# Kernel tuning notes

Hardware: AMD Instinct MI355X
Metric: run time of the kernel (lower is better)

Reference implementation:

```python
import jax, jax.numpy as jnp
import numpy as np

HEADS = 8
DIM_HEAD = 64

def setup_inputs() -> dict:
    key = jax.random.key(0)
    k1, k2, k3 = jax.random.split(key, 3)
    B, L, D = 8, 4096, 512
    hidden = HEADS * DIM_HEAD  # 512
    x = jax.random.normal(k1, (B, L, D), dtype=jnp.float32)
    # Conv1d(kernel_size=1) weights, squeezed to 2D matrices
    Wqkv = jax.random.normal(k2, (3 * hidden, D), dtype=jnp.float32) * (1.0 / np.sqrt(D))
    Wout = jax.random.normal(k3, (D, hidden), dtype=jnp.float32) * (1.0 / np.sqrt(hidden))
    bout = jnp.zeros((D,), dtype=jnp.float32)
    return {"x": x, "Wqkv": Wqkv, "Wout": Wout, "bout": bout}

def reference(x, Wqkv, Wout, bout):
    B, L, D = x.shape
    H, C = HEADS, DIM_HEAD
    # pointwise conv == linear over channel dim: (b, 3*H*C, l)
    qkv = jnp.einsum('bld,od->bol', x, Wqkv)
    qkv = qkv.reshape(B, 3, H, C, L)  # channel split order: (qkv, heads, c)
    q, k, v = qkv[:, 0], qkv[:, 1], qkv[:, 2]  # each (b, h, c, l)
    k = jax.nn.softmax(k, axis=-1)   # softmax over sequence
    q = jax.nn.softmax(q, axis=-2)   # softmax over feature dim (q_norm=True)
    context = jnp.einsum('bhdn,bhen->bhde', k, v)   # (b,h,c,c)
    out = jnp.einsum('bhde,bhdn->bhen', context, q)  # (b,h,c,l)
    out = out.reshape(B, H * C, L)
    y = jnp.einsum('bcl,dc->bld', out, Wout) + bout  # to_out + permute back
    return y
```

## Files before the change

### kernel.cpp

```cpp
#include <hip/hip_runtime.h>

#define L 4096
#define D 512
#define NCH 16

typedef __bf16 bf16x8 __attribute__((ext_vector_type(8)));
typedef float  f32x4  __attribute__((ext_vector_type(4)));

__device__ __forceinline__ void load_lds16(const void* g, void* l) {
    __builtin_amdgcn_global_load_lds(
        (const __attribute__((address_space(1))) void*)g,
        (__attribute__((address_space(3))) void*)l, 16, 0, 0);
}

__device__ __forceinline__ void barrier_mem() {
    asm volatile("" ::: "memory");
    __builtin_amdgcn_s_barrier();
    asm volatile("" ::: "memory");
}

#define NX8  (8 * 4096 * 512 / 8)
#define NW18 (1536 * 512 / 8)
#define NW28 (512 * 512 / 8)
__global__ __launch_bounds__(256) void convert_all(const float* __restrict__ x,
                                                   const float* __restrict__ Wq,
                                                   const float* __restrict__ Wo,
                                                   __bf16* __restrict__ dst) {
    int i = blockIdx.x * 256 + threadIdx.x;
    if (i >= NX8 + NW18 + NW28) return;
    const float* s;
    if (i < NX8)             s = x  + (size_t)i * 8;
    else if (i < NX8 + NW18) s = Wq + (size_t)(i - NX8) * 8;
    else                     s = Wo + (size_t)(i - NX8 - NW18) * 8;
    float4 a = ((const float4*)s)[0], b = ((const float4*)s)[1];
    bf16x8 o = {(__bf16)a.x, (__bf16)a.y, (__bf16)a.z, (__bf16)a.w,
                (__bf16)b.x, (__bf16)b.y, (__bf16)b.z, (__bf16)b.w};
    *(bf16x8*)(dst + (size_t)i * 8) = o;
}

template <int M, int N, int K, typename CT>
__global__ __launch_bounds__(256, 2) void gemm_bf16_256x128(
    const __bf16* __restrict__ A, size_t aStride,
    const __bf16* __restrict__ B, size_t bStride,
    CT* __restrict__ C, size_t cStride,
    const float* __restrict__ bias) {
    __shared__ __align__(16) __bf16 sA[3][256 * 32];
    __shared__ __align__(16) __bf16 sB[3][128 * 32];
    constexpr int NQ = K / 32;
    const int b  = blockIdx.z;
    const int m0 = blockIdx.y * 256;
    const int n0 = blockIdx.x * 128;
    const int t    = threadIdx.x;
    const int wave = t >> 6, lane = t & 63;
    const int wm = (wave >> 1) * 128;
    const int wn = (wave & 1) * 64;
    const int fr = lane & 15, g = lane >> 4;
    const __bf16* Ab = A + (size_t)b * aStride + (size_t)m0 * K;
    const __bf16* Bb = B + (size_t)b * bStride + (size_t)n0 * K;
    CT* Cb = C + (size_t)b * cStride;

    f32x4 acc[8][4];
#pragma unroll
    for (int i = 0; i < 8; i++)
#pragma unroll
        for (int j = 0; j < 4; j++) acc[i][j] = (f32x4)(0.0f);

    auto stageA = [&](int q, __bf16* slot) {
#pragma unroll
        for (int it = 0; it < 4; ++it) {
            const int gi = it * 256 + t;
            const int row = gi >> 2, cc = gi & 3;
            const int scc = cc ^ ((row >> 1) & 3);
            load_lds16(Ab + (size_t)row * K + q * 32 + scc * 8, slot + gi * 8);
        }
    };
    auto stageB = [&](int q, __bf16* slot) {
#pragma unroll
        for (int it = 0; it < 2; ++it) {
            const int gi = it * 256 + t;
            const int row = gi >> 2, cc = gi & 3;
            const int scc = cc ^ ((row >> 1) & 3);
            load_lds16(Bb + (size_t)row * K + q * 32 + scc * 8, slot + gi * 8);
        }
    };
    auto rdFrag = [&](const __bf16* slot, int rowbase) -> bf16x8 {
        const int row = rowbase + fr;
        return *(const bf16x8*)&slot[row * 32 + ((g ^ ((row >> 1) & 3)) * 8)];
    };

    stageB(0, sB[0]); stageA(0, sA[0]);
    stageB(1, sB[1]); stageA(1, sA[1]);

    for (int q = 0; q < NQ; ++q) {
        const int sl = q % 3;
        if (q < NQ - 1) asm volatile("s_waitcnt vmcnt(6)" ::: "memory");
        else            asm volatile("s_waitcnt vmcnt(0)" ::: "memory");
        barrier_mem();
        if (q + 2 < NQ) {
            const int ss = (q + 2) % 3;
            stageB(q + 2, sB[ss]);
            stageA(q + 2, sA[ss]);
        }
        bf16x8 fB[4], fA[8];
#pragma unroll
        for (int j = 0; j < 4; ++j) fB[j] = rdFrag(sB[sl], wn + j * 16);
#pragma unroll
        for (int i = 0; i < 8; ++i) fA[i] = rdFrag(sA[sl], wm + i * 16);
        asm volatile("s_waitcnt lgkmcnt(0)" ::: "memory");
        __builtin_amdgcn_sched_barrier(0);
        __builtin_amdgcn_s_setprio(1);
#pragma unroll
        for (int i = 0; i < 8; ++i)
#pragma unroll
            for (int j = 0; j < 4; ++j)
                acc[i][j] = __builtin_amdgcn_mfma_f32_16x16x32_bf16(
                    fA[i], fB[j], acc[i][j], 0, 0, 0);
        __builtin_amdgcn_s_setprio(0);
    }

    const int rb = g * 4;
    float bv[4];
#pragma unroll
    for (int j = 0; j < 4; ++j) bv[j] = bias ? bias[n0 + wn + j * 16 + fr] : 0.0f;
#pragma unroll
    for (int i = 0; i < 8; ++i) {
#pragma unroll
        for (int r = 0; r < 4; ++r) {
            const int m = m0 + wm + i * 16 + rb + r;
            CT* rowp = Cb + (size_t)m * N + n0 + wn + fr;
#pragma unroll
            for (int j = 0; j < 4; ++j)
                rowp[j * 16] = (CT)(acc[i][j][r] + bv[j]);
        }
    }
}

__global__ __launch_bounds__(256) void kstats(const __bf16* __restrict__ qkv,
                                              float2* __restrict__ stats) {
    const int r = blockIdx.x;
    const int b = r >> 9, hc = r & 511;
    const __bf16* row = qkv + (size_t)b * 1536 * L + (size_t)(512 + hc) * L;
    __shared__ float sred[4];
    const int t = threadIdx.x;
    const bf16x8* p = (const bf16x8*)row;
    bf16x8 c0 = p[t * 2], c1 = p[t * 2 + 1];
    float v[16];
    float m = -1e30f;
#pragma unroll
    for (int j = 0; j < 8; j++) {
        v[j] = (float)c0[j];
        v[8 + j] = (float)c1[j];
    }
#pragma unroll
    for (int j = 0; j < 16; j++) m = fmaxf(m, v[j]);
#pragma unroll
    for (int off = 32; off > 0; off >>= 1) m = fmaxf(m, __shfl_down(m, off, 64));
    if ((t & 63) == 0) sred[t >> 6] = m;
    __syncthreads();
    const float m4 = fmaxf(fmaxf(sred[0], sred[1]), fmaxf(sred[2], sred[3]));
    float s = 0.f;
#pragma unroll
    for (int j = 0; j < 16; j++) s += __expf(v[j] - m4);
#pragma unroll
    for (int off = 32; off > 0; off >>= 1) s += __shfl_down(s, off, 64);
    __syncthreads();
    if ((t & 63) == 0) sred[t >> 6] = s;
    __syncthreads();
    if (t == 0) {
        const float stot = sred[0] + sred[1] + sred[2] + sred[3];
        stats[r] = make_float2(m4, 1.0f / stot);
    }
}

#define SKS 264
__global__ __launch_bounds__(256) void context_mfma(const __bf16* __restrict__ qkv,
                                                    const float2* __restrict__ stats,
                                                    float* __restrict__ ctxp) {
    __shared__ __align__(16) __bf16 smem[2 * 64 * SKS];
    __shared__ float smax[64];
    __bf16* sk = smem;
    __bf16* sv = smem + 64 * SKS;
    const int chunk = blockIdx.x;
    const int bh = blockIdx.y;
    const int b = bh >> 3, h = bh & 7;
    const __bf16* kbase = qkv + (size_t)b * 1536 * L + (size_t)(512 + h * 64) * L;
    const __bf16* vbase = qkv + (size_t)b * 1536 * L + (size_t)(1024 + h * 64) * L;
    const int t = threadIdx.x;
    if (t < 64) smax[t] = stats[bh * 64 + t].x;
    __syncthreads();

    {
        const int d = t >> 2, noff = (t & 3) * 64;
        const int n0 = chunk * 256;
        const __bf16* kp = kbase + (size_t)d * L + n0 + noff;
        const __bf16* vp = vbase + (size_t)d * L + n0 + noff;
        const float md = smax[d];
#pragma unroll
        for (int c = 0; c < 8; c++) {
            bf16x8 kk = *(const bf16x8*)(kp + c * 8);
            bf16x8 vv = *(const bf16x8*)(vp + c * 8);
            bf16x8 ek;
#pragma unroll
            for (int j = 0; j < 8; j++) ek[j] = (__bf16)__expf((float)kk[j] - md);
            *(bf16x8*)&sk[d * SKS + noff + c * 8] = ek;
            *(bf16x8*)&sv[d * SKS + noff + c * 8] = vv;
        }
    }
    __syncthreads();

    const int wave = t >> 6, lane = t & 63;
    const int fr = lane & 15, kq = (lane >> 4) * 8;
    f32x4 acc[4][4];
#pragma unroll
    for (int i = 0; i < 4; i++)
#pragma unroll
        for (int j = 0; j < 4; j++) acc[i][j] = (f32x4)(0.0f);
#pragma unroll
    for (int kh = 0; kh < 2; kh++) {
        const int koff = wave * 64 + kh * 32 + kq;
        bf16x8 af[4], bfr[4];
#pragma unroll
        for (int i = 0; i < 4; i++) {
            af[i]  = *(const bf16x8*)&sk[(i * 16 + fr) * SKS + koff];
            bfr[i] = *(const bf16x8*)&sv[(i * 16 + fr) * SKS + koff];
        }
#pragma unroll
        for (int i = 0; i < 4; i++)
#pragma unroll
            for (int j = 0; j < 4; j++)
                acc[i][j] = __builtin_amdgcn_mfma_f32_16x16x32_bf16(af[i], bfr[j], acc[i][j], 0, 0, 0);
    }
    __syncthreads();

    float* red = (float*)smem;
    const int col = lane & 15, rbase = (lane >> 4) * 4;
#pragma unroll
    for (int i = 0; i < 4; i++)
#pragma unroll
        for (int j = 0; j < 4; j++)
#pragma unroll
            for (int r = 0; r < 4; r++) {
                const int dd = i * 16 + rbase + r;
                const int ee = j * 16 + col;
                red[wave * 4096 + dd * 64 + ee] = acc[i][j][r];
            }
    __syncthreads();
    float* cp = ctxp + ((size_t)chunk * 64 + bh) * 4096;
#pragma unroll
    for (int gg = 0; gg < 4; gg++) {
        const int idx = t * 16 + gg * 4;
        f32x4 s = *(const f32x4*)&red[idx];
        s += *(const f32x4*)&red[4096 + idx];
        s += *(const f32x4*)&red[8192 + idx];
        s += *(const f32x4*)&red[12288 + idx];
        *(f32x4*)&cp[idx] = s;
    }
}

__global__ __launch_bounds__(256) void ctx_reduce(const float* __restrict__ ctxp,
                                                  const float2* __restrict__ stats,
                                                  __bf16* __restrict__ ctxT) {
    const int bh = blockIdx.x >> 2, quarter = blockIdx.x & 3;
    const int t = threadIdx.x;
    const int flat = quarter * 1024 + t * 4;
    const int d = flat >> 6, e0 = flat & 63;
    f32x4 s = (f32x4)(0.0f);
    for (int ch = 0; ch < NCH; ch++)
        s += *(const f32x4*)&ctxp[((size_t)ch * 64 + bh) * 4096 + flat];
    const float inv = stats[bh * 64 + d].y;
    __bf16* o = ctxT + (size_t)bh * 4096;
#pragma unroll
    for (int j = 0; j < 4; j++) o[(e0 + j) * 64 + d] = (__bf16)(s[j] * inv);
}

#define SPS 66
__global__ __launch_bounds__(256) void pv_fused(__bf16* __restrict__ qkv,
                                                const __bf16* __restrict__ ctxT) {
    __shared__ __align__(16) __bf16 sp[256 * SPS];
    __shared__ __align__(16) __bf16 sctx[64 * SPS];
    __shared__ float sinv[256];
    const int tileN = blockIdx.x;
    const int bh = blockIdx.y;
    const int b = bh >> 3, h = bh & 7;
    const int t = threadIdx.x;
    const int n0 = tileN * 256;
    const __bf16* qbase = qkv + (size_t)b * 1536 * L + (size_t)(h * 64) * L;

    {
        const int e = t >> 2, c = t & 3;
        const bf16x8* src = (const bf16x8*)(ctxT + ((size_t)bh * 64 + e) * 64 + c * 16);
        *(bf16x8*)&sctx[e * SPS + c * 16] = src[0];
        *(bf16x8*)&sctx[e * SPS + c * 16 + 8] = src[1];
    }

    float m = -1e30f;
    float qv[64];
#pragma unroll
    for (int d = 0; d < 64; d++) {
        qv[d] = (float)qbase[(size_t)d * L + n0 + t];
        m = fmaxf(m, qv[d]);
    }
    float s = 0.f;
#pragma unroll
    for (int d0 = 0; d0 < 64; d0 += 8) {
        bf16x8 ek;
#pragma unroll
        for (int j = 0; j < 8; j++) {
            float e = __expf(qv[d0 + j] - m);
            s += e;
            ek[j] = (__bf16)e;
        }
        *(bf16x8*)&sp[t * SPS + d0] = ek;
    }
    sinv[t] = 1.0f / s;
    __syncthreads();

    const int wave = t >> 6, lane = t & 63;
    const int wm = wave * 64;
    const int fr = lane & 15, kq = (lane >> 4) * 8;
    f32x4 acc[4][4];
#pragma unroll
    for (int i = 0; i < 4; i++)
#pragma unroll
        for (int j = 0; j < 4; j++) acc[i][j] = (f32x4)(0.0f);
#pragma unroll
    for (int kh = 0; kh < 2; kh++) {
        bf16x8 af[4], bfr[4];
#pragma unroll
        for (int i = 0; i < 4; i++)
            af[i] = *(const bf16x8*)&sp[(wm + i * 16 + fr) * SPS + kh * 32 + kq];
#pragma unroll
        for (int j = 0; j < 4; j++)
            bfr[j] = *(const bf16x8*)&sctx[(j * 16 + fr) * SPS + kh * 32 + kq];
#pragma unroll
        for (int i = 0; i < 4; i++)
#pragma unroll
            for (int j = 0; j < 4; j++)
                acc[i][j] = __builtin_amdgcn_mfma_f32_16x16x32_bf16(af[i], bfr[j], acc[i][j], 0, 0, 0);
    }

    __bf16* ob = qkv + (size_t)b * 1536 * L + (size_t)512 * L;
    const int col = lane & 15, rbase = (lane >> 4) * 4;
#pragma unroll
    for (int i = 0; i < 4; i++) {
#pragma unroll
        for (int r = 0; r < 4; r++) {
            const int nl = wm + i * 16 + rbase + r;
            const float inv = sinv[nl];
            const size_t rowoff = (size_t)(n0 + nl) * 512 + h * 64;
#pragma unroll
            for (int j = 0; j < 4; j++)
                ob[rowoff + j * 16 + col] = (__bf16)(acc[i][j][r] * inv);
        }
    }
}

extern "C" void kernel_launch(void* const* d_in, const int* in_sizes, int n_in,
                              void* d_out, int out_size, void* d_ws, size_t ws_size,
                              hipStream_t stream) {
    const float* x    = (const float*)d_in[0];
    const float* Wqkv = (const float*)d_in[1];
    const float* Wout = (const float*)d_in[2];
    const float* bout = (const float*)d_in[3];
    float* y = (float*)d_out;

    __bf16* qkv   = (__bf16*)d_ws;
    float*  ctxp  = (float*)(qkv + (size_t)8 * 1536 * L);
    __bf16* xb    = (__bf16*)(ctxp + (size_t)NCH * 64 * 4096);
    __bf16* Wqb   = xb + (size_t)8 * 4096 * 512;
    __bf16* Wob   = Wqb + (size_t)1536 * 512;
    float2* stats = (float2*)(Wob + (size_t)512 * 512);
    __bf16* ctxT  = (__bf16*)(stats + 4096);

    const int convBlocks = (NX8 + NW18 + NW28 + 255) / 256;
    convert_all<<<dim3(convBlocks), 256, 0, stream>>>(x, Wqkv, Wout, xb);

    gemm_bf16_256x128<1536, 4096, 512, __bf16><<<dim3(4096 / 128, 1536 / 256, 8), 256, 0, stream>>>(
        Wqb, 0, xb, (size_t)4096 * 512, qkv, (size_t)1536 * 4096, nullptr);

    kstats<<<dim3(4096), 256, 0, stream>>>(qkv, stats);
    context_mfma<<<dim3(NCH, 64), 256, 0, stream>>>(qkv, stats, ctxp);
    ctx_reduce<<<dim3(256), 256, 0, stream>>>(ctxp, stats, ctxT);
    pv_fused<<<dim3(L / 256, 64), 256, 0, stream>>>(qkv, ctxT);

    const __bf16* outT = qkv + (size_t)512 * L;
    gemm_bf16_256x128<4096, 512, 512, float><<<dim3(512 / 128, 4096 / 256, 8), 256, 0, stream>>>(
        outT, (size_t)1536 * L, Wob, 0, y, (size_t)4096 * 512, bout);
}
```

Baseline: 267.8 us.

## Double-buffer A fragments in registers and precompute GEMM load addresses

The bf16 GEMM now loads the next K-slice's A fragments from LDS into a second register buffer while the current slice's MFMAs run, so LDS read latency overlaps with compute. Global-to-LDS source pointers and LDS fragment offsets are computed once before the loop instead of every iteration, and the K loop is fully unrolled. In exchange, each iteration now waits for all outstanding global loads (vmcnt(0)) instead of keeping one extra slice in flight, which reduces how far global prefetch runs ahead. The doubled A fragment buffers also raise register pressure.

Result: no change. 266.8 us (-0.4%).

```diff
diff --git a/kernel.cpp b/kernel.cpp
--- a/kernel.cpp
+++ b/kernel.cpp
@@ -39,13 +39,13 @@
 }
 
 template <int M, int N, int K, typename CT>
-__global__ __launch_bounds__(256, 2) void gemm_bf16_256x128(
+__global__ __launch_bounds__(256, 2) void gemm_bf16_pipe(
     const __bf16* __restrict__ A, size_t aStride,
     const __bf16* __restrict__ B, size_t bStride,
     CT* __restrict__ C, size_t cStride,
     const float* __restrict__ bias) {
+    __shared__ __align__(16) __bf16 sB[3][128 * 32];
     __shared__ __align__(16) __bf16 sA[3][256 * 32];
-    __shared__ __align__(16) __bf16 sB[3][128 * 32];
     constexpr int NQ = K / 32;
     const int b  = blockIdx.z;
     const int m0 = blockIdx.y * 256;
@@ -59,54 +59,65 @@
     const __bf16* Bb = B + (size_t)b * bStride + (size_t)n0 * K;
     CT* Cb = C + (size_t)b * cStride;
 
+    const __bf16* pA_[4];
+    const __bf16* pB_[2];
+#pragma unroll
+    for (int it = 0; it < 4; ++it) {
+        const int gi = it * 256 + t, row = gi >> 2, cc = gi & 3;
+        pA_[it] = Ab + (size_t)row * K + (cc ^ ((row >> 1) & 3)) * 8;
+    }
+#pragma unroll
+    for (int it = 0; it < 2; ++it) {
+        const int gi = it * 256 + t, row = gi >> 2, cc = gi & 3;
+        pB_[it] = Bb + (size_t)row * K + (cc ^ ((row >> 1) & 3)) * 8;
+    }
+    const int lchunk = (g ^ ((fr >> 1) & 3)) * 8;
+    const int laneA = (wm + fr) * 32 + lchunk;
+    const int laneB = (wn + fr) * 32 + lchunk;
+
     f32x4 acc[8][4];
 #pragma unroll
     for (int i = 0; i < 8; i++)
 #pragma unroll
         for (int j = 0; j < 4; j++) acc[i][j] = (f32x4)(0.0f);
 
-    auto stageA = [&](int q, __bf16* slot) {
-#pragma unroll
-        for (int it = 0; it < 4; ++it) {
-            const int gi = it * 256 + t;
-            const int row = gi >> 2, cc = gi & 3;
-            const int scc = cc ^ ((row >> 1) & 3);
-            load_lds16(Ab + (size_t)row * K + q * 32 + scc * 8, slot + gi * 8);
-        }
+    auto stagePair = [&](int q, int sl) {
+#pragma unroll
+        for (int it = 0; it < 4; ++it)
+            load_lds16(pA_[it] + q * 32, &sA[sl][(it * 256 + t) * 8]);
+#pragma unroll
+        for (int it = 0; it < 2; ++it)
+            load_lds16(pB_[it] + q * 32, &sB[sl][(it * 256 + t) * 8]);
     };
-    auto stageB = [&](int q, __bf16* slot) {
-#pragma unroll
-        for (int it = 0; it < 2; ++it) {
-            const int gi = it * 256 + t;
-            const int row = gi >> 2, cc = gi & 3;
-            const int scc = cc ^ ((row >> 1) & 3);
-            load_lds16(Bb + (size_t)row * K + q * 32 + scc * 8, slot + gi * 8);
-        }
-    };
-    auto rdFrag = [&](const __bf16* slot, int rowbase) -> bf16x8 {
-        const int row = rowbase + fr;
-        return *(const bf16x8*)&slot[row * 32 + ((g ^ ((row >> 1) & 3)) * 8)];
-    };
-
-    stageB(0, sB[0]); stageA(0, sA[0]);
-    stageB(1, sB[1]); stageA(1, sA[1]);
-
+
+    bf16x8 fA0[8], fA1[8], fB[4];
+
+    stagePair(0, 0);
+    stagePair(1, 1);
+    asm volatile("s_waitcnt vmcnt(6)" ::: "memory");
+    barrier_mem();
+#pragma unroll
+    for (int i = 0; i < 8; ++i)
+        fA0[i] = *(const bf16x8*)&sA[0][laneA + i * 512];
+
+#pragma unroll
     for (int q = 0; q < NQ; ++q) {
-        const int sl = q % 3;
-        if (q < NQ - 1) asm volatile("s_waitcnt vmcnt(6)" ::: "memory");
-        else            asm volatile("s_waitcnt vmcnt(0)" ::: "memory");
+        asm volatile("s_waitcnt vmcnt(0)" ::: "memory");
         barrier_mem();
-        if (q + 2 < NQ) {
-            const int ss = (q + 2) % 3;
-            stageB(q + 2, sB[ss]);
-            stageA(q + 2, sA[ss]);
-        }
-        bf16x8 fB[4], fA[8];
-#pragma unroll
-        for (int j = 0; j < 4; ++j) fB[j] = rdFrag(sB[sl], wn + j * 16);
-#pragma unroll
-        for (int i = 0; i < 8; ++i) fA[i] = rdFrag(sA[sl], wm + i * 16);
-        asm volatile("s_waitcnt lgkmcnt(0)" ::: "memory");
+        if (q + 2 < NQ) stagePair(q + 2, (q + 2) % 3);
+#pragma unroll
+        for (int j = 0; j < 4; ++j)
+            fB[j] = *(const bf16x8*)&sB[q % 3][laneB + j * 512];
+        bf16x8* fAc = (q & 1) ? fA1 : fA0;
+        bf16x8* fAn = (q & 1) ? fA0 : fA1;
+        if (q + 1 < NQ) {
+#pragma unroll
+            for (int i = 0; i < 8; ++i)
+                fAn[i] = *(const bf16x8*)&sA[(q + 1) % 3][laneA + i * 512];
+            asm volatile("s_waitcnt lgkmcnt(8)" ::: "memory");
+        } else {
+            asm volatile("s_waitcnt lgkmcnt(0)" ::: "memory");
+        }
         __builtin_amdgcn_sched_barrier(0);
         __builtin_amdgcn_s_setprio(1);
 #pragma unroll
@@ -114,7 +125,7 @@
 #pragma unroll
             for (int j = 0; j < 4; ++j)
                 acc[i][j] = __builtin_amdgcn_mfma_f32_16x16x32_bf16(
-                    fA[i], fB[j], acc[i][j], 0, 0, 0);
+                    fAc[i], fB[j], acc[i][j], 0, 0, 0);
         __builtin_amdgcn_s_setprio(0);
     }
 
@@ -375,7 +386,7 @@
     const int convBlocks = (NX8 + NW18 + NW28 + 255) / 256;
     convert_all<<<dim3(convBlocks), 256, 0, stream>>>(x, Wqkv, Wout, xb);
 
-    gemm_bf16_256x128<1536, 4096, 512, __bf16><<<dim3(4096 / 128, 1536 / 256, 8), 256, 0, stream>>>(
+    gemm_bf16_pipe<1536, 4096, 512, __bf16><<<dim3(4096 / 128, 1536 / 256, 8), 256, 0, stream>>>(
         Wqb, 0, xb, (size_t)4096 * 512, qkv, (size_t)1536 * 4096, nullptr);
 
     kstats<<<dim3(4096), 256, 0, stream>>>(qkv, stats);
@@ -384,6 +395,6 @@
     pv_fused<<<dim3(L / 256, 64), 256, 0, stream>>>(qkv, ctxT);
 
     const __bf16* outT = qkv + (size_t)512 * L;
-    gemm_bf16_256x128<4096, 512, 512, float><<<dim3(512 / 128, 4096 / 256, 8), 256, 0, stream>>>(
+    gemm_bf16_pipe<4096, 512, 512, float><<<dim3(512 / 128, 4096 / 256, 8), 256, 0, stream>>>(
         outT, (size_t)1536 * L, Wob, 0, y, (size_t)4096 * 512, bout);
 }
```
